# Kernel tuning notes

Hardware: AMD Instinct MI355X
Metric: run time of the kernel (lower is better)

Reference implementation:

```python
import jax, jax.numpy as jnp
import numpy as np

TRI_PLANE_AXES = np.array([
    [[1, 0, 0], [0, 1, 0], [0, 0, 1]],
    [[1, 0, 0], [0, 0, 1], [0, 1, 0]],
    [[0, 0, 1], [0, 1, 0], [1, 0, 0]],
], dtype=np.float32)


def _grid_sample_bilinear(img, ix, iy):
    # img: [C,H,W]; ix, iy: [M] unnormalized pixel coords.
    # Matches torch grid_sample(mode='bilinear', padding_mode='zeros', align_corners=False).
    C, H, W = img.shape
    x0f = jnp.floor(ix)
    y0f = jnp.floor(iy)
    wx = ix - x0f
    wy = iy - y0f
    x0 = x0f.astype(jnp.int32)
    y0 = y0f.astype(jnp.int32)

    def gather(yi, xi):
        valid = (xi >= 0) & (xi < W) & (yi >= 0) & (yi < H)
        v = img[:, jnp.clip(yi, 0, H - 1), jnp.clip(xi, 0, W - 1)]  # [C,M]
        return v * valid.astype(img.dtype)

    v00 = gather(y0, x0)
    v01 = gather(y0, x0 + 1)
    v10 = gather(y0 + 1, x0)
    v11 = gather(y0 + 1, x0 + 1)
    return (v00 * (1 - wy) * (1 - wx) + v01 * (1 - wy) * wx
            + v10 * wy * (1 - wx) + v11 * wy * wx)  # [C,M]


def setup_inputs() -> dict:
    key = jax.random.key(0)
    k1, k2 = jax.random.split(key)
    N, M = 4, 131072
    C, S = 64, 512
    coords = jax.random.uniform(k1, (N, M, 3), jnp.float32, minval=-1.0, maxval=1.0)
    tplanes = jax.random.uniform(k2, (1, 3, C, S, S), jnp.float32, minval=-0.01, maxval=0.01)
    return {"coords": coords, "tplanes": tplanes}


def reference(coords, tplanes):
    N, M, _ = coords.shape
    _, n_planes, C, H, W = tplanes.shape
    inv_planes = jnp.linalg.inv(jnp.asarray(TRI_PLANE_AXES))  # [3,3,3] (tiny)
    # projections[..., :2]: coords @ inv_plane per plane
    proj = jnp.einsum('nmc,pcd->npmd', coords, inv_planes)[..., :2]  # [N,3,M,2]
    gx, gy = proj[..., 0], proj[..., 1]
    # align_corners=False unnormalization
    ix = ((gx + 1.0) * W - 1.0) * 0.5
    iy = ((gy + 1.0) * H - 1.0) * 0.5
    imgs = jnp.broadcast_to(tplanes, (N, n_planes, C, H, W)).reshape(N * n_planes, C, H, W)
    feats = jax.vmap(_grid_sample_bilinear)(
        imgs, ix.reshape(N * n_planes, M), iy.reshape(N * n_planes, M))  # [N*3,C,M]
    feats = feats.reshape(N, n_planes, C, M).transpose(0, 3, 1, 2)  # [N,M,3,C]
    return feats.reshape(N, M, n_planes * C)  # concat over planes
```

## Files before the change

### kernel.cpp

```cpp
#include <hip/hip_runtime.h>
#include <hip/hip_fp16.h>

namespace {

constexpr int S = 512;
constexpr int C = 64;
constexpr int TILE = 16;
constexpr int TPP  = 32;
constexpr int NBINS = 3 * TPP * TPP;
constexpr int CAP = 744;
constexpr int OVF_CAP = 8192;
constexpr int BIN_IT = 4;

constexpr int HH = 17;
constexpr int HW = 17;
constexpr int TSTRIDE = 68;
constexpr int LDSH = HH * HW * TSTRIDE;

typedef float f32x4 __attribute__((ext_vector_type(4)));
struct alignas(8) H4 { __half2 a, b; };
typedef unsigned long long u64;

__device__ __forceinline__ unsigned quantg(float g)
{
    float v = (g + 1.0f) * 262144.0f;
    int q = (int)floorf(v);
    q = min(max(q, 0), 1048575);
    return (unsigned)q;
}

__device__ __forceinline__ int x0_of_q(unsigned q) { return ((int)q - 512) >> 10; }

__device__ __forceinline__ int bin_from_q(int p, unsigned qx, unsigned qy)
{
    int xc0 = min(max(x0_of_q(qx), 0), S - 1);
    int yc0 = min(max(x0_of_q(qy), 0), S - 1);
    return p * (TPP * TPP) + (yc0 >> 4) * TPP + (xc0 >> 4);
}

__global__ __launch_bounds__(512) void tp_bin(const float* __restrict__ coords,
                                              int total_s,
                                              int* __restrict__ bincnt,
                                              u64* __restrict__ slots,
                                              u64* __restrict__ ovf,
                                              int* __restrict__ ovf_cnt)
{
    __shared__ int lh[NBINS];
    __shared__ int lbase[NBINS];
    int t = threadIdx.x;
    for (int i = t; i < NBINS; i += 512) lh[i] = 0;
    __syncthreads();
    int base = blockIdx.x * (512 * BIN_IT);

    int  bn [BIN_IT][3];
    u64  rec[BIN_IT][3];

    #pragma unroll
    for (int it = 0; it < BIN_IT; ++it) {
        int s = base + it * 512 + t;
        #pragma unroll
        for (int p = 0; p < 3; ++p) bn[it][p] = -1;
        if (s < total_s) {
            float cx = coords[3 * s], cy = coords[3 * s + 1], cz = coords[3 * s + 2];
            #pragma unroll
            for (int p = 0; p < 3; ++p) {
                float gx = (p == 2) ? cz : cx;
                float gy = (p == 1) ? cz : cy;
                unsigned qx = quantg(gx), qy = quantg(gy);
                int b = bin_from_q(p, qx, qy);
                bn[it][p]  = b;
                rec[it][p] = ((u64)(3 * s + p) << 40) | ((u64)qy << 20) | qx;
                atomicAdd(&lh[b], 1);
            }
        }
    }
    __syncthreads();
    for (int i = t; i < NBINS; i += 512) {
        int c = lh[i];
        if (c) lbase[i] = atomicAdd(&bincnt[i], c);
    }
    __syncthreads();
    for (int i = t; i < NBINS; i += 512) lh[i] = 0;
    __syncthreads();

    #pragma unroll
    for (int it = 0; it < BIN_IT; ++it) {
        #pragma unroll
        for (int p = 0; p < 3; ++p) {
            int b = bn[it][p];
            if (b >= 0) {
                int r = atomicAdd(&lh[b], 1);
                int slot = lbase[b] + r;
                if (slot < CAP) {
                    slots[(size_t)b * CAP + slot] = rec[it][p];
                } else {
                    int o = atomicAdd(ovf_cnt, 1);
                    if (o < OVF_CAP) ovf[o] = rec[it][p];
                }
            }
        }
    }
}

__global__ __launch_bounds__(512) void tp_sample_tiled(const float* __restrict__ tp,
                                                       const int* __restrict__ bincnt,
                                                       const u64* __restrict__ slots,
                                                       const u64* __restrict__ ovf,
                                                       const int* __restrict__ ovf_cnt,
                                                       float* __restrict__ out)
{
    __shared__ __half tile[LDSH] __attribute__((aligned(16)));

    int b0i = blockIdx.x;
    int b = (b0i & 7) * (NBINS / 8) + (b0i >> 3);

    int p  = b >> 10;
    int ty = (b >> 5) & 31;
    int tx = b & 31;
    int xg = tx * TILE;
    int yg = ty * TILE;

    const float* pl = tp + (size_t)p * C * (S * S);

    for (int task = threadIdx.x; task < C * HH * 5; task += 512) {
        int seg = task % 5;
        int rem = task / 5;
        int row = rem % HH;
        int ch  = rem / HH;
        int y   = min(yg + row, S - 1);
        int cb  = (seg < 4) ? seg * 4 : 13;
        int xb  = xg + cb;
        if (xb > S - 4) xb = S - 4;
        float4 v = *reinterpret_cast<const float4*>(pl + ((size_t)ch * S + y) * S + xb);
        __half* trow = &tile[(row * HW) * TSTRIDE + ch];
        #pragma unroll
        for (int i = 0; i < 4; ++i) {
            int col = xb + i - xg;
            if (col >= 0 && col < HW)
                trow[col * TSTRIDE] = __float2half(((const float*)&v)[i]);
        }
        if (xb != xg + cb)
            trow[16 * TSTRIDE] = __float2half(((const float*)&v)[3]);
    }
    __syncthreads();

    int cnt = min(bincnt[b], CAP);
    const u64* sb = slots + (size_t)b * CAP;
    int grp = threadIdx.x >> 3;
    int t   = threadIdx.x & 7;

    for (int gi = grp; gi < cnt; gi += 64) {
        u64 rec = sb[gi];
        int sp = (int)(rec >> 40);
        unsigned qx = (unsigned)rec & 0xFFFFFu;
        unsigned qy = (unsigned)(rec >> 20) & 0xFFFFFu;

        float ix = (float)qx * (1.0f / 1024.0f) - 0.5f;
        float iy = (float)qy * (1.0f / 1024.0f) - 0.5f;
        int x0 = x0_of_q(qx), y0 = x0_of_q(qy);
        float wx = ix - (float)x0, wy = iy - (float)y0;
        int x1 = x0 + 1, y1 = y0 + 1;

        bool vx0 = ((unsigned)x0 < (unsigned)S);
        bool vx1 = ((unsigned)x1 < (unsigned)S);
        bool vy0 = ((unsigned)y0 < (unsigned)S);
        bool vy1 = ((unsigned)y1 < (unsigned)S);

        float w00 = (vx0 && vy0) ? (1.0f - wy) * (1.0f - wx) : 0.0f;
        float w01 = (vx1 && vy0) ? (1.0f - wy) * wx          : 0.0f;
        float w10 = (vx0 && vy1) ? wy * (1.0f - wx)          : 0.0f;
        float w11 = (vx1 && vy1) ? wy * wx                   : 0.0f;

        int lx0 = min(max(x0, 0), S - 1) - xg;
        int lx1 = min(max(x1, 0), S - 1) - xg;
        int ly0 = min(max(y0, 0), S - 1) - yg;
        int ly1 = min(max(y1, 0), S - 1) - yg;

        int o00 = (ly0 * HW + lx0) * TSTRIDE;
        int o01 = (ly0 * HW + lx1) * TSTRIDE;
        int o10 = (ly1 * HW + lx0) * TSTRIDE;
        int o11 = (ly1 * HW + lx1) * TSTRIDE;

        #pragma unroll
        for (int h = 0; h < 2; ++h) {
            int c = 4 * t + 32 * h;
            H4 v00 = *reinterpret_cast<const H4*>(&tile[o00 + c]);
            H4 v01 = *reinterpret_cast<const H4*>(&tile[o01 + c]);
            H4 v10 = *reinterpret_cast<const H4*>(&tile[o10 + c]);
            H4 v11 = *reinterpret_cast<const H4*>(&tile[o11 + c]);

            float2 a  = __half22float2(v00.a), a2 = __half22float2(v00.b);
            float2 bb = __half22float2(v01.a), b2 = __half22float2(v01.b);
            float2 cc = __half22float2(v10.a), c2 = __half22float2(v10.b);
            float2 d  = __half22float2(v11.a), d2 = __half22float2(v11.b);

            f32x4 r;
            r.x = w00 * a.x  + w01 * bb.x + w10 * cc.x + w11 * d.x;
            r.y = w00 * a.y  + w01 * bb.y + w10 * cc.y + w11 * d.y;
            r.z = w00 * a2.x + w01 * b2.x + w10 * c2.x + w11 * d2.x;
            r.w = w00 * a2.y + w01 * b2.y + w10 * c2.y + w11 * d2.y;

            __builtin_nontemporal_store(r, reinterpret_cast<f32x4*>(out + (size_t)sp * 64 + c));
        }
    }

    if (b0i == 0) {
        int ocnt = min(*ovf_cnt, OVF_CAP);
        for (int e = grp; e < ocnt; e += 64) {
            u64 rec = ovf[e];
            int sp = (int)(rec >> 40);
            unsigned qx = (unsigned)rec & 0xFFFFFu;
            unsigned qy = (unsigned)(rec >> 20) & 0xFFFFFu;
            int pp = sp - 3 * (sp / 3);

            float ix = (float)qx * (1.0f / 1024.0f) - 0.5f;
            float iy = (float)qy * (1.0f / 1024.0f) - 0.5f;
            int x0 = x0_of_q(qx), y0 = x0_of_q(qy);
            float wx = ix - (float)x0, wy = iy - (float)y0;
            int x1 = x0 + 1, y1 = y0 + 1;

            bool vx0 = ((unsigned)x0 < (unsigned)S);
            bool vx1 = ((unsigned)x1 < (unsigned)S);
            bool vy0 = ((unsigned)y0 < (unsigned)S);
            bool vy1 = ((unsigned)y1 < (unsigned)S);

            float w00 = (vx0 && vy0) ? (1.0f - wy) * (1.0f - wx) : 0.0f;
            float w01 = (vx1 && vy0) ? (1.0f - wy) * wx          : 0.0f;
            float w10 = (vx0 && vy1) ? wy * (1.0f - wx)          : 0.0f;
            float w11 = (vx1 && vy1) ? wy * wx                   : 0.0f;

            int xc0 = min(max(x0, 0), S - 1), xc1 = min(max(x1, 0), S - 1);
            int yc0 = min(max(y0, 0), S - 1), yc1 = min(max(y1, 0), S - 1);

            int o00 = yc0 * S + xc0, o01 = yc0 * S + xc1;
            int o10 = yc1 * S + xc0, o11 = yc1 * S + xc1;

            const float* pb = tp + (size_t)pp * C * (S * S);
            #pragma unroll
            for (int h = 0; h < 2; ++h) {
                float r[4];
                #pragma unroll
                for (int j = 0; j < 4; ++j) {
                    const float* ch = pb + (size_t)(4 * t + 32 * h + j) * (S * S);
                    r[j] = w00 * ch[o00] + w01 * ch[o01] + w10 * ch[o10] + w11 * ch[o11];
                }
                float4 v = make_float4(r[0], r[1], r[2], r[3]);
                *reinterpret_cast<float4*>(out + (size_t)sp * 64 + 4 * t + 32 * h) = v;
            }
        }
    }
}

__global__ __launch_bounds__(256) void tp_sample_direct(const float* __restrict__ coords,
                                                        const float* __restrict__ tp,
                                                        float* __restrict__ out,
                                                        int total_sp)
{
    int tid = blockIdx.x * 256 + threadIdx.x;
    int gi = tid >> 4;
    if (gi >= total_sp) return;
    int t = tid & 15;

    int s = gi / 3;
    int p = gi - 3 * s;
    float cx = coords[3 * s], cy = coords[3 * s + 1], cz = coords[3 * s + 2];
    float gx = (p == 2) ? cz : cx;
    float gy = (p == 1) ? cz : cy;
    float ix = (gx + 1.0f) * 256.0f - 0.5f;
    float iy = (gy + 1.0f) * 256.0f - 0.5f;

    float x0f = floorf(ix), y0f = floorf(iy);
    float wx = ix - x0f, wy = iy - y0f;
    int x0 = (int)x0f, y0 = (int)y0f;
    int x1 = x0 + 1,   y1 = y0 + 1;

    bool vx0 = ((unsigned)x0 < (unsigned)S);
    bool vx1 = ((unsigned)x1 < (unsigned)S);
    bool vy0 = ((unsigned)y0 < (unsigned)S);
    bool vy1 = ((unsigned)y1 < (unsigned)S);

    float w00 = (vx0 && vy0) ? (1.0f - wy) * (1.0f - wx) : 0.0f;
    float w01 = (vx1 && vy0) ? (1.0f - wy) * wx          : 0.0f;
    float w10 = (vx0 && vy1) ? wy * (1.0f - wx)          : 0.0f;
    float w11 = (vx1 && vy1) ? wy * wx                   : 0.0f;

    int xc0 = min(max(x0, 0), S - 1), xc1 = min(max(x1, 0), S - 1);
    int yc0 = min(max(y0, 0), S - 1), yc1 = min(max(y1, 0), S - 1);

    int o00 = yc0 * S + xc0, o01 = yc0 * S + xc1;
    int o10 = yc1 * S + xc0, o11 = yc1 * S + xc1;

    const float* pb = tp + (size_t)p * C * (S * S);
    float r[4];
    #pragma unroll
    for (int j = 0; j < 4; ++j) {
        const float* ch = pb + (size_t)(4 * t + j) * (S * S);
        r[j] = w00 * ch[o00] + w01 * ch[o01] + w10 * ch[o10] + w11 * ch[o11];
    }
    float4 v = make_float4(r[0], r[1], r[2], r[3]);
    *reinterpret_cast<float4*>(out + (size_t)gi * 64 + 4 * t) = v;
}

}

extern "C" void kernel_launch(void* const* d_in, const int* in_sizes, int n_in,
                              void* d_out, int out_size, void* d_ws, size_t ws_size,
                              hipStream_t stream)
{
    const float* coords  = (const float*)d_in[0];
    const float* tplanes = (const float*)d_in[1];
    float* out = (float*)d_out;

    int total_sp = in_sizes[0];
    int total_s  = total_sp / 3;

    const size_t bincntOff = 0;
    const size_t ovfcntOff = (size_t)NBINS * 4;
    const size_t ovfOff    = 12352;
    const size_t slotsOff  = ovfOff + (size_t)OVF_CAP * 8;
    const size_t need      = slotsOff + (size_t)NBINS * CAP * 8;

    if (ws_size >= need) {
        int* bincnt  = (int*)((char*)d_ws + bincntOff);
        int* ovf_cnt = (int*)((char*)d_ws + ovfcntOff);
        u64* ovf     = (u64*)((char*)d_ws + ovfOff);
        u64* slots   = (u64*)((char*)d_ws + slotsOff);

        int nb_bin = (total_s + 512 * BIN_IT - 1) / (512 * BIN_IT);

        hipMemsetAsync(d_ws, 0, ovfcntOff + 64, stream);
        tp_bin<<<nb_bin, 512, 0, stream>>>(coords, total_s, bincnt, slots, ovf, ovf_cnt);
        tp_sample_tiled<<<NBINS, 512, 0, stream>>>(tplanes, bincnt, slots, ovf, ovf_cnt, out);
    } else {
        int nb_sm = (total_sp * 16 + 255) / 256;
        tp_sample_direct<<<nb_sm, 256, 0, stream>>>(coords, tplanes, out, total_sp);
    }
}
```

Measured before the change: 133.0 us.

## Fuse binning and tiled sampling into one cooperative persistent kernel

Merges the binning pass and the tiled sampling pass into a single cooperative kernel of 768 persistent blocks. Each block bins its share of coordinates, prefetches its first halo tile before a grid-wide sync, then processes four bins serially, reusing one LDS buffer for both the histogram and the tile. This removes one kernel launch and overlaps the first tile load with the binning wait. The cost is a grid barrier, fewer and serial bins per block with less latency hiding, and reliance on cooperative launch residency, with the old two-kernel path kept as a fallback.

```diff
diff --git a/kernel.cpp b/kernel.cpp
--- a/kernel.cpp
+++ b/kernel.cpp
@@ -1,5 +1,8 @@
 #include <hip/hip_runtime.h>
 #include <hip/hip_fp16.h>
+#include <hip/hip_cooperative_groups.h>
+
+namespace cg = cooperative_groups;
 
 namespace {
 
@@ -10,7 +13,9 @@
 constexpr int NBINS = 3 * TPP * TPP;
 constexpr int CAP = 744;
 constexpr int OVF_CAP = 8192;
-constexpr int BIN_IT = 4;
+
+constexpr int GRID_BLOCKS = 768;
+constexpr int BINS_PER_BLOCK = 4;
 
 constexpr int HH = 17;
 constexpr int HW = 17;
@@ -37,6 +42,253 @@
     int yc0 = min(max(x0_of_q(qy), 0), S - 1);
     return p * (TPP * TPP) + (yc0 >> 4) * TPP + (xc0 >> 4);
 }
+
+__device__ __forceinline__ void halo_load(const float* __restrict__ tp, int bin,
+                                          __half* __restrict__ tile)
+{
+    int p  = bin >> 10;
+    int ty = (bin >> 5) & 31;
+    int tx = bin & 31;
+    int xg = tx * TILE;
+    int yg = ty * TILE;
+    const float* pl = tp + (size_t)p * C * (S * S);
+
+    for (int task = threadIdx.x; task < C * HH * 5; task += 512) {
+        int seg = task % 5;
+        int rem = task / 5;
+        int row = rem % HH;
+        int ch  = rem / HH;
+        int y   = min(yg + row, S - 1);
+        int cb  = (seg < 4) ? seg * 4 : 13;
+        int xb  = xg + cb;
+        if (xb > S - 4) xb = S - 4;
+        float4 v = *reinterpret_cast<const float4*>(pl + ((size_t)ch * S + y) * S + xb);
+        __half* trow = &tile[(row * HW) * TSTRIDE + ch];
+        #pragma unroll
+        for (int i = 0; i < 4; ++i) {
+            int col = xb + i - xg;
+            if (col >= 0 && col < HW)
+                trow[col * TSTRIDE] = __float2half(((const float*)&v)[i]);
+        }
+        if (xb != xg + cb)
+            trow[16 * TSTRIDE] = __float2half(((const float*)&v)[3]);
+    }
+}
+
+__device__ __forceinline__ void sample_bin(int bin, int cnt,
+                                           const u64* __restrict__ sb,
+                                           const __half* __restrict__ tile,
+                                           float* __restrict__ out)
+{
+    int xg = (bin & 31) * TILE;
+    int yg = ((bin >> 5) & 31) * TILE;
+    int grp = threadIdx.x >> 3;
+    int t   = threadIdx.x & 7;
+
+    for (int gi = grp; gi < cnt; gi += 64) {
+        u64 rec = sb[gi];
+        int sp = (int)(rec >> 40);
+        unsigned qx = (unsigned)rec & 0xFFFFFu;
+        unsigned qy = (unsigned)(rec >> 20) & 0xFFFFFu;
+
+        float ix = (float)qx * (1.0f / 1024.0f) - 0.5f;
+        float iy = (float)qy * (1.0f / 1024.0f) - 0.5f;
+        int x0 = x0_of_q(qx), y0 = x0_of_q(qy);
+        float wx = ix - (float)x0, wy = iy - (float)y0;
+        int x1 = x0 + 1, y1 = y0 + 1;
+
+        bool vx0 = ((unsigned)x0 < (unsigned)S);
+        bool vx1 = ((unsigned)x1 < (unsigned)S);
+        bool vy0 = ((unsigned)y0 < (unsigned)S);
+        bool vy1 = ((unsigned)y1 < (unsigned)S);
+
+        float w00 = (vx0 && vy0) ? (1.0f - wy) * (1.0f - wx) : 0.0f;
+        float w01 = (vx1 && vy0) ? (1.0f - wy) * wx          : 0.0f;
+        float w10 = (vx0 && vy1) ? wy * (1.0f - wx)          : 0.0f;
+        float w11 = (vx1 && vy1) ? wy * wx                   : 0.0f;
+
+        int lx0 = min(max(x0, 0), S - 1) - xg;
+        int lx1 = min(max(x1, 0), S - 1) - xg;
+        int ly0 = min(max(y0, 0), S - 1) - yg;
+        int ly1 = min(max(y1, 0), S - 1) - yg;
+
+        int o00 = (ly0 * HW + lx0) * TSTRIDE;
+        int o01 = (ly0 * HW + lx1) * TSTRIDE;
+        int o10 = (ly1 * HW + lx0) * TSTRIDE;
+        int o11 = (ly1 * HW + lx1) * TSTRIDE;
+
+        #pragma unroll
+        for (int h = 0; h < 2; ++h) {
+            int c = 4 * t + 32 * h;
+            H4 v00 = *reinterpret_cast<const H4*>(&tile[o00 + c]);
+            H4 v01 = *reinterpret_cast<const H4*>(&tile[o01 + c]);
+            H4 v10 = *reinterpret_cast<const H4*>(&tile[o10 + c]);
+            H4 v11 = *reinterpret_cast<const H4*>(&tile[o11 + c]);
+
+            float2 a  = __half22float2(v00.a), a2 = __half22float2(v00.b);
+            float2 bb = __half22float2(v01.a), b2 = __half22float2(v01.b);
+            float2 cc = __half22float2(v10.a), c2 = __half22float2(v10.b);
+            float2 d  = __half22float2(v11.a), d2 = __half22float2(v11.b);
+
+            f32x4 r;
+            r.x = w00 * a.x  + w01 * bb.x + w10 * cc.x + w11 * d.x;
+            r.y = w00 * a.y  + w01 * bb.y + w10 * cc.y + w11 * d.y;
+            r.z = w00 * a2.x + w01 * b2.x + w10 * c2.x + w11 * d2.x;
+            r.w = w00 * a2.y + w01 * b2.y + w10 * c2.y + w11 * d2.y;
+
+            __builtin_nontemporal_store(r, reinterpret_cast<f32x4*>(out + (size_t)sp * 64 + c));
+        }
+    }
+}
+
+__device__ __forceinline__ void ovf_drain(const float* __restrict__ tp,
+                                          const u64* __restrict__ ovf,
+                                          const int* __restrict__ ovf_cnt,
+                                          float* __restrict__ out)
+{
+    int grp = threadIdx.x >> 3;
+    int t   = threadIdx.x & 7;
+    int ocnt = min(*ovf_cnt, OVF_CAP);
+    for (int e = grp; e < ocnt; e += 64) {
+        u64 rec = ovf[e];
+        int sp = (int)(rec >> 40);
+        unsigned qx = (unsigned)rec & 0xFFFFFu;
+        unsigned qy = (unsigned)(rec >> 20) & 0xFFFFFu;
+        int pp = sp - 3 * (sp / 3);
+
+        float ix = (float)qx * (1.0f / 1024.0f) - 0.5f;
+        float iy = (float)qy * (1.0f / 1024.0f) - 0.5f;
+        int x0 = x0_of_q(qx), y0 = x0_of_q(qy);
+        float wx = ix - (float)x0, wy = iy - (float)y0;
+        int x1 = x0 + 1, y1 = y0 + 1;
+
+        bool vx0 = ((unsigned)x0 < (unsigned)S);
+        bool vx1 = ((unsigned)x1 < (unsigned)S);
+        bool vy0 = ((unsigned)y0 < (unsigned)S);
+        bool vy1 = ((unsigned)y1 < (unsigned)S);
+
+        float w00 = (vx0 && vy0) ? (1.0f - wy) * (1.0f - wx) : 0.0f;
+        float w01 = (vx1 && vy0) ? (1.0f - wy) * wx          : 0.0f;
+        float w10 = (vx0 && vy1) ? wy * (1.0f - wx)          : 0.0f;
+        float w11 = (vx1 && vy1) ? wy * wx                   : 0.0f;
+
+        int xc0 = min(max(x0, 0), S - 1), xc1 = min(max(x1, 0), S - 1);
+        int yc0 = min(max(y0, 0), S - 1), yc1 = min(max(y1, 0), S - 1);
+
+        int o00 = yc0 * S + xc0, o01 = yc0 * S + xc1;
+        int o10 = yc1 * S + xc0, o11 = yc1 * S + xc1;
+
+        const float* pb = tp + (size_t)pp * C * (S * S);
+        #pragma unroll
+        for (int h = 0; h < 2; ++h) {
+            float r[4];
+            #pragma unroll
+            for (int j = 0; j < 4; ++j) {
+                const float* ch = pb + (size_t)(4 * t + 32 * h + j) * (S * S);
+                r[j] = w00 * ch[o00] + w01 * ch[o01] + w10 * ch[o10] + w11 * ch[o11];
+            }
+            float4 v = make_float4(r[0], r[1], r[2], r[3]);
+            *reinterpret_cast<float4*>(out + (size_t)sp * 64 + 4 * t + 32 * h) = v;
+        }
+    }
+}
+
+__global__ __launch_bounds__(512, 6) void tp_fused(const float* __restrict__ tp,
+                                                   const float* __restrict__ coords,
+                                                   int total_s, int share,
+                                                   int* __restrict__ bincnt,
+                                                   u64* __restrict__ slots,
+                                                   u64* __restrict__ ovf,
+                                                   int* __restrict__ ovf_cnt,
+                                                   float* __restrict__ out)
+{
+    __shared__ __align__(16) unsigned char smem_raw[LDSH * 2];
+    int*    lh    = reinterpret_cast<int*>(smem_raw);
+    int*    lbase = reinterpret_cast<int*>(smem_raw + NBINS * 4);
+    __half* tile  = reinterpret_cast<__half*>(smem_raw);
+
+    int t = threadIdx.x;
+    int blk = blockIdx.x;
+    int stripe = blk & 7;
+    int off    = blk >> 3;
+
+    for (int i = t; i < NBINS; i += 512) lh[i] = 0;
+    __syncthreads();
+
+    int base_s = blk * share;
+    int send   = min(base_s + share, total_s);
+
+    int bn [2][3];
+    u64 rec[2][3];
+
+    #pragma unroll
+    for (int it = 0; it < 2; ++it) {
+        int s = base_s + it * 512 + t;
+        #pragma unroll
+        for (int p = 0; p < 3; ++p) bn[it][p] = -1;
+        if (s < send) {
+            float cx = coords[3 * s], cy = coords[3 * s + 1], cz = coords[3 * s + 2];
+            #pragma unroll
+            for (int p = 0; p < 3; ++p) {
+                float gx = (p == 2) ? cz : cx;
+                float gy = (p == 1) ? cz : cy;
+                unsigned qx = quantg(gx), qy = quantg(gy);
+                int b = bin_from_q(p, qx, qy);
+                bn[it][p]  = b;
+                rec[it][p] = ((u64)(3 * s + p) << 40) | ((u64)qy << 20) | qx;
+                atomicAdd(&lh[b], 1);
+            }
+        }
+    }
+    __syncthreads();
+    for (int i = t; i < NBINS; i += 512) {
+        int c = lh[i];
+        int gb = 0;
+        if (c) gb = atomicAdd(&bincnt[i], c);
+        lbase[i] = gb;
+        lh[i] = 0;
+    }
+    __syncthreads();
+    #pragma unroll
+    for (int it = 0; it < 2; ++it) {
+        #pragma unroll
+        for (int p = 0; p < 3; ++p) {
+            int b = bn[it][p];
+            if (b >= 0) {
+                int r = atomicAdd(&lh[b], 1);
+                int slot = lbase[b] + r;
+                if (slot < CAP) {
+                    slots[(size_t)b * CAP + slot] = rec[it][p];
+                } else {
+                    int o = atomicAdd(ovf_cnt, 1);
+                    if (o < OVF_CAP) ovf[o] = rec[it][p];
+                }
+            }
+        }
+    }
+    __syncthreads();
+
+    int bin0 = stripe * (NBINS / 8) + off;
+    halo_load(tp, bin0, tile);
+
+    cg::this_grid().sync();
+
+    #pragma unroll
+    for (int k = 0; k < BINS_PER_BLOCK; ++k) {
+        int bin = stripe * (NBINS / 8) + off + k * (GRID_BLOCKS / 8);
+        if (k > 0) {
+            __syncthreads();
+            halo_load(tp, bin, tile);
+        }
+        __syncthreads();
+        int cnt = min(bincnt[bin], CAP);
+        sample_bin(bin, cnt, slots + (size_t)bin * CAP, tile, out);
+    }
+
+    if (blk == 0) ovf_drain(tp, ovf, ovf_cnt, out);
+}
+
+constexpr int FB_BIN_IT = 2;
 
 __global__ __launch_bounds__(512) void tp_bin(const float* __restrict__ coords,
                                               int total_s,
@@ -50,13 +302,13 @@
     int t = threadIdx.x;
     for (int i = t; i < NBINS; i += 512) lh[i] = 0;
     __syncthreads();
-    int base = blockIdx.x * (512 * BIN_IT);
-
-    int  bn [BIN_IT][3];
-    u64  rec[BIN_IT][3];
-
-    #pragma unroll
-    for (int it = 0; it < BIN_IT; ++it) {
+    int base = blockIdx.x * (512 * FB_BIN_IT);
+
+    int bn [FB_BIN_IT][3];
+    u64 rec[FB_BIN_IT][3];
+
+    #pragma unroll
+    for (int it = 0; it < FB_BIN_IT; ++it) {
         int s = base + it * 512 + t;
         #pragma unroll
         for (int p = 0; p < 3; ++p) bn[it][p] = -1;
@@ -77,14 +329,14 @@
     __syncthreads();
     for (int i = t; i < NBINS; i += 512) {
         int c = lh[i];
-        if (c) lbase[i] = atomicAdd(&bincnt[i], c);
-    }
-    __syncthreads();
-    for (int i = t; i < NBINS; i += 512) lh[i] = 0;
-    __syncthreads();
-
-    #pragma unroll
-    for (int it = 0; it < BIN_IT; ++it) {
+        int gb = 0;
+        if (c) gb = atomicAdd(&bincnt[i], c);
+        lbase[i] = gb;
+        lh[i] = 0;
+    }
+    __syncthreads();
+    #pragma unroll
+    for (int it = 0; it < FB_BIN_IT; ++it) {
         #pragma unroll
         for (int p = 0; p < 3; ++p) {
             int b = bn[it][p];
@@ -114,141 +366,13 @@
     int b0i = blockIdx.x;
     int b = (b0i & 7) * (NBINS / 8) + (b0i >> 3);
 
-    int p  = b >> 10;
-    int ty = (b >> 5) & 31;
-    int tx = b & 31;
-    int xg = tx * TILE;
-    int yg = ty * TILE;
-
-    const float* pl = tp + (size_t)p * C * (S * S);
-
-    for (int task = threadIdx.x; task < C * HH * 5; task += 512) {
-        int seg = task % 5;
-        int rem = task / 5;
-        int row = rem % HH;
-        int ch  = rem / HH;
-        int y   = min(yg + row, S - 1);
-        int cb  = (seg < 4) ? seg * 4 : 13;
-        int xb  = xg + cb;
-        if (xb > S - 4) xb = S - 4;
-        float4 v = *reinterpret_cast<const float4*>(pl + ((size_t)ch * S + y) * S + xb);
-        __half* trow = &tile[(row * HW) * TSTRIDE + ch];
-        #pragma unroll
-        for (int i = 0; i < 4; ++i) {
-            int col = xb + i - xg;
-            if (col >= 0 && col < HW)
-                trow[col * TSTRIDE] = __float2half(((const float*)&v)[i]);
-        }
-        if (xb != xg + cb)
-            trow[16 * TSTRIDE] = __float2half(((const float*)&v)[3]);
-    }
+    halo_load(tp, b, tile);
     __syncthreads();
 
     int cnt = min(bincnt[b], CAP);
-    const u64* sb = slots + (size_t)b * CAP;
-    int grp = threadIdx.x >> 3;
-    int t   = threadIdx.x & 7;
-
-    for (int gi = grp; gi < cnt; gi += 64) {
-        u64 rec = sb[gi];
-        int sp = (int)(rec >> 40);
-        unsigned qx = (unsigned)rec & 0xFFFFFu;
-        unsigned qy = (unsigned)(rec >> 20) & 0xFFFFFu;
-
-        float ix = (float)qx * (1.0f / 1024.0f) - 0.5f;
-        float iy = (float)qy * (1.0f / 1024.0f) - 0.5f;
-        int x0 = x0_of_q(qx), y0 = x0_of_q(qy);
-        float wx = ix - (float)x0, wy = iy - (float)y0;
-        int x1 = x0 + 1, y1 = y0 + 1;
-
-        bool vx0 = ((unsigned)x0 < (unsigned)S);
-        bool vx1 = ((unsigned)x1 < (unsigned)S);
-        bool vy0 = ((unsigned)y0 < (unsigned)S);
-        bool vy1 = ((unsigned)y1 < (unsigned)S);
-
-        float w00 = (vx0 && vy0) ? (1.0f - wy) * (1.0f - wx) : 0.0f;
-        float w01 = (vx1 && vy0) ? (1.0f - wy) * wx          : 0.0f;
-        float w10 = (vx0 && vy1) ? wy * (1.0f - wx)          : 0.0f;
-        float w11 = (vx1 && vy1) ? wy * wx                   : 0.0f;
-
-        int lx0 = min(max(x0, 0), S - 1) - xg;
-        int lx1 = min(max(x1, 0), S - 1) - xg;
-        int ly0 = min(max(y0, 0), S - 1) - yg;
-        int ly1 = min(max(y1, 0), S - 1) - yg;
-
-        int o00 = (ly0 * HW + lx0) * TSTRIDE;
-        int o01 = (ly0 * HW + lx1) * TSTRIDE;
-        int o10 = (ly1 * HW + lx0) * TSTRIDE;
-        int o11 = (ly1 * HW + lx1) * TSTRIDE;
-
-        #pragma unroll
-        for (int h = 0; h < 2; ++h) {
-            int c = 4 * t + 32 * h;
-            H4 v00 = *reinterpret_cast<const H4*>(&tile[o00 + c]);
-            H4 v01 = *reinterpret_cast<const H4*>(&tile[o01 + c]);
-            H4 v10 = *reinterpret_cast<const H4*>(&tile[o10 + c]);
-            H4 v11 = *reinterpret_cast<const H4*>(&tile[o11 + c]);
-
-            float2 a  = __half22float2(v00.a), a2 = __half22float2(v00.b);
-            float2 bb = __half22float2(v01.a), b2 = __half22float2(v01.b);
-            float2 cc = __half22float2(v10.a), c2 = __half22float2(v10.b);
-            float2 d  = __half22float2(v11.a), d2 = __half22float2(v11.b);
-
-            f32x4 r;
-            r.x = w00 * a.x  + w01 * bb.x + w10 * cc.x + w11 * d.x;
-            r.y = w00 * a.y  + w01 * bb.y + w10 * cc.y + w11 * d.y;
-            r.z = w00 * a2.x + w01 * b2.x + w10 * c2.x + w11 * d2.x;
-            r.w = w00 * a2.y + w01 * b2.y + w10 * c2.y + w11 * d2.y;
-
-            __builtin_nontemporal_store(r, reinterpret_cast<f32x4*>(out + (size_t)sp * 64 + c));
-        }
-    }
-
-    if (b0i == 0) {
-        int ocnt = min(*ovf_cnt, OVF_CAP);
-        for (int e = grp; e < ocnt; e += 64) {
-            u64 rec = ovf[e];
-            int sp = (int)(rec >> 40);
-            unsigned qx = (unsigned)rec & 0xFFFFFu;
-            unsigned qy = (unsigned)(rec >> 20) & 0xFFFFFu;
-            int pp = sp - 3 * (sp / 3);
-
-            float ix = (float)qx * (1.0f / 1024.0f) - 0.5f;
-            float iy = (float)qy * (1.0f / 1024.0f) - 0.5f;
-            int x0 = x0_of_q(qx), y0 = x0_of_q(qy);
-            float wx = ix - (float)x0, wy = iy - (float)y0;
-            int x1 = x0 + 1, y1 = y0 + 1;
-
-            bool vx0 = ((unsigned)x0 < (unsigned)S);
-            bool vx1 = ((unsigned)x1 < (unsigned)S);
-            bool vy0 = ((unsigned)y0 < (unsigned)S);
-            bool vy1 = ((unsigned)y1 < (unsigned)S);
-
-            float w00 = (vx0 && vy0) ? (1.0f - wy) * (1.0f - wx) : 0.0f;
-            float w01 = (vx1 && vy0) ? (1.0f - wy) * wx          : 0.0f;
-            float w10 = (vx0 && vy1) ? wy * (1.0f - wx)          : 0.0f;
-            float w11 = (vx1 && vy1) ? wy * wx                   : 0.0f;
-
-            int xc0 = min(max(x0, 0), S - 1), xc1 = min(max(x1, 0), S - 1);
-            int yc0 = min(max(y0, 0), S - 1), yc1 = min(max(y1, 0), S - 1);
-
-            int o00 = yc0 * S + xc0, o01 = yc0 * S + xc1;
-            int o10 = yc1 * S + xc0, o11 = yc1 * S + xc1;
-
-            const float* pb = tp + (size_t)pp * C * (S * S);
-            #pragma unroll
-            for (int h = 0; h < 2; ++h) {
-                float r[4];
-                #pragma unroll
-                for (int j = 0; j < 4; ++j) {
-                    const float* ch = pb + (size_t)(4 * t + 32 * h + j) * (S * S);
-                    r[j] = w00 * ch[o00] + w01 * ch[o01] + w10 * ch[o10] + w11 * ch[o11];
-                }
-                float4 v = make_float4(r[0], r[1], r[2], r[3]);
-                *reinterpret_cast<float4*>(out + (size_t)sp * 64 + 4 * t + 32 * h) = v;
-            }
-        }
-    }
+    sample_bin(b, cnt, slots + (size_t)b * CAP, tile, out);
+
+    if (b0i == 0) ovf_drain(tp, ovf, ovf_cnt, out);
 }
 
 __global__ __launch_bounds__(256) void tp_sample_direct(const float* __restrict__ coords,
@@ -326,11 +450,26 @@
         u64* ovf     = (u64*)((char*)d_ws + ovfOff);
         u64* slots   = (u64*)((char*)d_ws + slotsOff);
 
-        int nb_bin = (total_s + 512 * BIN_IT - 1) / (512 * BIN_IT);
-
         hipMemsetAsync(d_ws, 0, ovfcntOff + 64, stream);
-        tp_bin<<<nb_bin, 512, 0, stream>>>(coords, total_s, bincnt, slots, ovf, ovf_cnt);
-        tp_sample_tiled<<<NBINS, 512, 0, stream>>>(tplanes, bincnt, slots, ovf, ovf_cnt, out);
+
+        int share = (total_s + GRID_BLOCKS - 1) / GRID_BLOCKS;
+        bool coop_ok = (share <= 1024);
+
+        hipError_t e = hipErrorUnknown;
+        if (coop_ok) {
+            void* args[] = { (void*)&tplanes, (void*)&coords, (void*)&total_s,
+                             (void*)&share, (void*)&bincnt, (void*)&slots,
+                             (void*)&ovf, (void*)&ovf_cnt, (void*)&out };
+            e = hipLaunchCooperativeKernel((const void*)tp_fused,
+                                           dim3(GRID_BLOCKS), dim3(512),
+                                           args, 0, stream);
+        }
+        if (e != hipSuccess) {
+            int nb_bin = (total_s + 512 * FB_BIN_IT - 1) / (512 * FB_BIN_IT);
+            tp_bin<<<nb_bin, 512, 0, stream>>>(coords, total_s, bincnt, slots, ovf, ovf_cnt);
+            tp_sample_tiled<<<NBINS, 512, 0, stream>>>(tplanes, bincnt, slots,
+                                                       ovf, ovf_cnt, out);
+        }
     } else {
         int nb_sm = (total_sp * 16 + 255) / 256;
         tp_sample_direct<<<nb_sm, 256, 0, stream>>>(coords, tplanes, out, total_sp);
```

New measurement: 282.5 us. +112.5%, slower.
